# Kernel optimization log

Measured on AMD Instinct MI355X. Metric: run time of the kernel, lower is better.

## Reference

```python
import jax, jax.numpy as jnp
import numpy as np

H = 2048      # hidden_dim
OUT = 8       # output_dim
DICT = 50000  # dict_len (DND capacity)
FDIM = 6      # function_dim
RDIM = 1      # rule_dim
IN = FDIM + RDIM + OUT + 1  # input_dim = 16
NG = 5        # N_GATES
EPS = 1e-8


def setup_inputs() -> dict:
    key = jax.random.key(0)
    ks = jax.random.split(key, 16)
    f = lambda i, shape, s=1.0: jax.random.normal(ks[i], shape, jnp.float32) * s
    return {
        "x_t": f(0, (1, IN)),
        "h": f(1, (1, 1, H), 0.1),
        "c": f(2, (1, 1, H), 0.1),
        "W_i2h": f(3, ((NG + 1) * H, IN), 0.05),
        "b_i2h": jnp.zeros(((NG + 1) * H,), jnp.float32),
        "W_h2h": f(4, ((NG + 1) * H, H), 0.02),
        "b_h2h": jnp.zeros(((NG + 1) * H,), jnp.float32),
        "f_keys": f(5, (DICT, FDIM)),
        "f_vals": f(6, (DICT, H), 0.1),
        "r_keys": f(7, (DICT, RDIM)),
        "r_vals": f(8, (DICT, H), 0.1),
        "W_ih": f(9, (H, H), 0.02),
        "b_ih": jnp.zeros((H,), jnp.float32),
        "W_actor": f(10, (OUT, H), 0.02),
        "b_actor": jnp.zeros((OUT,), jnp.float32),
        "W_critic": f(11, (1, H), 0.02),
        "b_critic": jnp.zeros((1,), jnp.float32),
        "write_idx": 12345,
    }


def _dnd_read(q, keys, vals):
    # cosine similarity between query q [d] and all keys [N, d], softmax policy,
    # weighted sum over stored values [N, H] -> [H]
    qn = q / (jnp.linalg.norm(q) + EPS)
    kn = keys / (jnp.linalg.norm(keys, axis=1, keepdims=True) + EPS)
    sim = kn @ qn                      # [N]
    w = jax.nn.softmax(sim)            # [N]
    return w @ vals                    # [H]


def reference(x_t, h, c, W_i2h, b_i2h, W_h2h, b_h2h,
              f_keys, f_vals, r_keys, r_vals,
              W_ih, b_ih, W_actor, b_actor, W_critic, b_critic,
              write_idx):
    h2 = h.reshape(1, H)
    c2 = c.reshape(1, H)

    # fused gate preactivations: [1, 6H]
    preact = x_t @ W_i2h.T + b_i2h + h2 @ W_h2h.T + b_h2h
    gates = jax.nn.sigmoid(preact[:, :NG * H])
    f_t = gates[:, 0 * H:1 * H]
    i_t = gates[:, 1 * H:2 * H]
    o_t = gates[:, 2 * H:3 * H]
    fun_t = gates[:, 3 * H:4 * H]
    rul_t = gates[:, 4 * H:5 * H]
    c_new = jnp.tanh(preact[:, NG * H:])

    c_t = f_t * c2 + i_t * c_new

    # DND content-addressable reads (cosine sim + softmax over memory slots)
    q_f = x_t[0, :FDIM]
    q_r = x_t[0, FDIM:FDIM + RDIM]
    memfun_t = jnp.tanh(_dnd_read(q_f, f_keys, f_vals))  # [H]
    memrul_t = jnp.tanh(_dnd_read(q_r, r_keys, r_vals))  # [H]

    c_t = c_t + fun_t * memfun_t + rul_t * memrul_t
    h_t = o_t * jnp.tanh(c_t)

    # memory write (no-grad in original): function half / rule half of c_t
    c_ft = jax.lax.stop_gradient(c_t[0].at[H // 2:].set(0.0))
    c_rt = jax.lax.stop_gradient(c_t[0].at[:H // 2].set(0.0))
    new_f_keys = f_keys.at[write_idx].set(q_f)
    new_f_vals = f_vals.at[write_idx].set(c_ft)
    new_r_keys = r_keys.at[write_idx].set(q_r)
    new_r_vals = r_vals.at[write_idx].set(c_rt)

    # A2C head: shared relu layer, actor softmax, critic scalar
    ha = jax.nn.relu(h_t @ W_ih.T + b_ih)
    pi_a_t = jax.nn.softmax(ha @ W_actor.T + b_actor, axis=-1)  # [1, OUT]
    v_t = ha @ W_critic.T + b_critic                            # [1, 1]

    h_out = h_t.reshape(1, 1, H)
    c_out = c_t.reshape(1, 1, H)
    return (pi_a_t, v_t, h_out, c_out,
            new_f_keys, new_f_vals, new_r_keys, new_r_vals)
```

## Files before the change

### kernel.cpp

```cpp
#include <hip/hip_runtime.h>
#include <math.h>

#define H        2048
#define HD       12288
#define DICT     50000
#define FDIM     6
#define RDIM     1
#define IN_DIM   16
#define EPS_F    1e-8f

#define OFF_PI   ((size_t)0)
#define OFF_V    ((size_t)8)
#define OFF_H    ((size_t)9)
#define OFF_C    ((size_t)2057)
#define OFF_FK   ((size_t)4105)
#define OFF_FV   ((size_t)304105)
#define OFF_RK   ((size_t)102704105)
#define OFF_RV   ((size_t)102754105)

struct F4U { float x, y, z, w; };

__device__ __forceinline__ float sigf(float v) { return 1.0f / (1.0f + expf(-v)); }

__global__ void k_zero(float* __restrict__ p, int n) {
    int i = blockIdx.x * 256 + threadIdx.x;
    if (i < n) p[i] = 0.0f;
}

__global__ __launch_bounds__(256) void k_preact(
    const float* __restrict__ W_h2h, const float* __restrict__ W_i2h,
    const float* __restrict__ b_h2h, const float* __restrict__ b_i2h,
    const float* __restrict__ h, const float* __restrict__ x,
    float* __restrict__ preact)
{
    int gid  = blockIdx.x * blockDim.x + threadIdx.x;
    int row  = gid >> 6;
    int lane = threadIdx.x & 63;
    if (row >= HD) return;
    const float4* Wv = (const float4*)(W_h2h + (size_t)row * H);
    const float4* hv = (const float4*)h;
    float acc = 0.0f;
#pragma unroll
    for (int k = 0; k < 8; ++k) {
        float4 w4 = Wv[lane + (k << 6)];
        float4 h4 = hv[lane + (k << 6)];
        acc += w4.x * h4.x + w4.y * h4.y + w4.z * h4.z + w4.w * h4.w;
    }
    if (lane < IN_DIM) acc += W_i2h[(size_t)row * IN_DIM + lane] * x[lane];
#pragma unroll
    for (int off = 32; off > 0; off >>= 1) acc += __shfl_down(acc, off);
    if (lane == 0) preact[row] = acc + b_h2h[row] + b_i2h[row];
}

__global__ __launch_bounds__(256) void k_sims(
    const float* __restrict__ f_keys, const float* __restrict__ r_keys,
    const float* __restrict__ x,
    float* __restrict__ ef, float* __restrict__ er,
    float* __restrict__ sums,
    float* __restrict__ out_fk, float* __restrict__ out_rk)
{
    __shared__ float red[4];
    const int i    = blockIdx.x * 256 + threadIdx.x;
    const int dict = blockIdx.y;
    float e = 0.0f;

    if (dict == 0) {
        float qn[FDIM]; float qs = 0.0f;
        for (int d = 0; d < FDIM; ++d) { float q = x[d]; qn[d] = q; qs += q * q; }
        float qi = 1.0f / (sqrtf(qs) + EPS_F);
        if (i < DICT) {
            float ks = 0.0f, dot = 0.0f;
            for (int d = 0; d < FDIM; ++d) {
                float kv = f_keys[(size_t)i * FDIM + d];
                out_fk[(size_t)i * FDIM + d] = kv;
                ks += kv * kv; dot += kv * qn[d];
            }
            float sim = (dot * qi) / (sqrtf(ks) + EPS_F);
            e = expf(sim);
            ef[i] = e;
        }
    } else {
        float q  = x[FDIM];
        float qn = q / (fabsf(q) + EPS_F);
        if (i < DICT) {
            float kv = r_keys[i];
            out_rk[i] = kv;
            float sim = (kv * qn) / (fabsf(kv) + EPS_F);
            e = expf(sim);
            er[i] = e;
        }
    }
#pragma unroll
    for (int off = 32; off > 0; off >>= 1) e += __shfl_down(e, off);
    if ((threadIdx.x & 63) == 0) red[threadIdx.x >> 6] = e;
    __syncthreads();
    if (threadIdx.x == 0)
        atomicAdd(&sums[dict], red[0] + red[1] + red[2] + red[3]);
}

#define ROWS_PER_CHUNK 125
__global__ __launch_bounds__(256) void k_copy_wsum(
    const float* __restrict__ f_vals, const float* __restrict__ r_vals,
    const float* __restrict__ wf, const float* __restrict__ wr,
    float* __restrict__ out_fv, float* __restrict__ out_rv,
    float* __restrict__ memfun, float* __restrict__ memrul)
{
    __shared__ float wl[ROWS_PER_CHUNK];
    const int tid    = threadIdx.x;
    const int chunk  = blockIdx.x;
    const int stripe = blockIdx.y;
    const int dict   = blockIdx.z;

    const float* vals = dict ? r_vals : f_vals;
    const float* w    = dict ? wr     : wf;
    float*       outv = dict ? out_rv : out_fv;
    float*       mem  = dict ? memrul : memfun;

    const int row0 = chunk * ROWS_PER_CHUNK;
    if (tid < ROWS_PER_CHUNK) wl[tid] = w[row0 + tid];
    __syncthreads();

    const int colf = stripe * 256 + tid;
    const float4* vv = (const float4*)vals;
    F4U*          ov = (F4U*)outv;

    float ax = 0.f, ay = 0.f, az = 0.f, aw = 0.f;
    size_t base = (size_t)row0 * 512 + colf;
#pragma unroll 5
    for (int i = 0; i < ROWS_PER_CHUNK; ++i) {
        float4 v = vv[base];
        F4U s; s.x = v.x; s.y = v.y; s.z = v.z; s.w = v.w;
        ov[base] = s;
        float wv = wl[i];
        ax += wv * v.x; ay += wv * v.y; az += wv * v.z; aw += wv * v.w;
        base += 512;
    }
    const int c = colf * 4;
    atomicAdd(&mem[c + 0], ax);
    atomicAdd(&mem[c + 1], ay);
    atomicAdd(&mem[c + 2], az);
    atomicAdd(&mem[c + 3], aw);
}

__global__ __launch_bounds__(256) void k_combine(
    const float* __restrict__ preact, const float* __restrict__ c_in,
    const float* __restrict__ memfun, const float* __restrict__ memrul,
    const float* __restrict__ sums,
    const float* __restrict__ x, const int* __restrict__ widx_p,
    float* __restrict__ out, float* __restrict__ ht_ws)
{
    const int j = blockIdx.x * 256 + threadIdx.x;
    if (j >= H) return;
    const int widx = *widx_p;
    const float invf = 1.0f / sums[0];
    const float invr = 1.0f / sums[1];

    float f_t   = sigf(preact[0 * H + j]);
    float i_t   = sigf(preact[1 * H + j]);
    float o_t   = sigf(preact[2 * H + j]);
    float fun_t = sigf(preact[3 * H + j]);
    float rul_t = sigf(preact[4 * H + j]);
    float c_new = tanhf(preact[5 * H + j]);

    float ct = f_t * c_in[j] + i_t * c_new
             + fun_t * tanhf(memfun[j] * invf) + rul_t * tanhf(memrul[j] * invr);
    float ht = o_t * tanhf(ct);

    out[OFF_H + j] = ht;
    out[OFF_C + j] = ct;
    ht_ws[j] = ht;

    out[OFF_FV + (size_t)widx * H + j] = (j < H / 2) ? ct : 0.0f;
    out[OFF_RV + (size_t)widx * H + j] = (j < H / 2) ? 0.0f : ct;
    if (j < FDIM)  out[OFF_FK + (size_t)widx * FDIM + j] = x[j];
    if (j == FDIM) out[OFF_RK + (size_t)widx] = x[FDIM];
}

__global__ __launch_bounds__(256) void k_hidden(
    const float* __restrict__ W_ih, const float* __restrict__ b_ih,
    const float* __restrict__ ht, float* __restrict__ ha)
{
    int gid  = blockIdx.x * blockDim.x + threadIdx.x;
    int row  = gid >> 6;
    int lane = threadIdx.x & 63;
    if (row >= H) return;
    const float4* Wv = (const float4*)(W_ih + (size_t)row * H);
    const float4* hv = (const float4*)ht;
    float acc = 0.0f;
#pragma unroll
    for (int k = 0; k < 8; ++k) {
        float4 w4 = Wv[lane + (k << 6)];
        float4 h4 = hv[lane + (k << 6)];
        acc += w4.x * h4.x + w4.y * h4.y + w4.z * h4.z + w4.w * h4.w;
    }
#pragma unroll
    for (int off = 32; off > 0; off >>= 1) acc += __shfl_down(acc, off);
    if (lane == 0) ha[row] = fmaxf(acc + b_ih[row], 0.0f);
}

__global__ __launch_bounds__(256) void k_heads(
    const float* __restrict__ W_actor, const float* __restrict__ b_actor,
    const float* __restrict__ W_critic, const float* __restrict__ b_critic,
    const float* __restrict__ ha, float* __restrict__ out)
{
    __shared__ float red[4];
    __shared__ float logits[9];
    const int tid = threadIdx.x;

    for (int o = 0; o < 9; ++o) {
        const float* row = (o < 8) ? (W_actor + (size_t)o * H) : W_critic;
        float acc = 0.0f;
        for (int k = tid; k < H; k += 256) acc += row[k] * ha[k];
#pragma unroll
        for (int off = 32; off > 0; off >>= 1) acc += __shfl_down(acc, off);
        if ((tid & 63) == 0) red[tid >> 6] = acc;
        __syncthreads();
        if (tid == 0)
            logits[o] = red[0] + red[1] + red[2] + red[3] + ((o < 8) ? b_actor[o] : b_critic[0]);
        __syncthreads();
    }
    if (tid == 0) {
        float m = logits[0];
        for (int o = 1; o < 8; ++o) m = fmaxf(m, logits[o]);
        float e[8], s = 0.0f;
        for (int o = 0; o < 8; ++o) { e[o] = expf(logits[o] - m); s += e[o]; }
        for (int o = 0; o < 8; ++o) out[OFF_PI + o] = e[o] / s;
        out[OFF_V] = logits[8];
    }
}

extern "C" void kernel_launch(void* const* d_in, const int* in_sizes, int n_in,
                              void* d_out, int out_size, void* d_ws, size_t ws_size,
                              hipStream_t stream)
{
    const float* x        = (const float*)d_in[0];
    const float* h        = (const float*)d_in[1];
    const float* c        = (const float*)d_in[2];
    const float* W_i2h    = (const float*)d_in[3];
    const float* b_i2h    = (const float*)d_in[4];
    const float* W_h2h    = (const float*)d_in[5];
    const float* b_h2h    = (const float*)d_in[6];
    const float* f_keys   = (const float*)d_in[7];
    const float* f_vals   = (const float*)d_in[8];
    const float* r_keys   = (const float*)d_in[9];
    const float* r_vals   = (const float*)d_in[10];
    const float* W_ih     = (const float*)d_in[11];
    const float* b_ih     = (const float*)d_in[12];
    const float* W_actor  = (const float*)d_in[13];
    const float* b_actor  = (const float*)d_in[14];
    const float* W_critic = (const float*)d_in[15];
    const float* b_critic = (const float*)d_in[16];
    const int*   widx     = (const int*)d_in[17];

    float* out = (float*)d_out;
    float* ws  = (float*)d_ws;

    float* preact = ws;
    float* ef     = ws + 12288;
    float* er     = ws + 62288;
    float* memfun = ws + 112288;
    float* memrul = ws + 114336;
    float* sums   = ws + 116384;
    float* ht_ws  = ws + 116392;
    float* ha     = ws + 118440;

    k_zero<<<17, 256, 0, stream>>>(memfun, 2 * H + 2);

    k_preact<<<HD / 4, 256, 0, stream>>>(W_h2h, W_i2h, b_h2h, b_i2h, h, x, preact);

    k_sims<<<dim3((DICT + 255) / 256, 2), 256, 0, stream>>>(
        f_keys, r_keys, x, ef, er, sums, out + OFF_FK, out + OFF_RK);

    k_copy_wsum<<<dim3(DICT / ROWS_PER_CHUNK, 2, 2), 256, 0, stream>>>(
        f_vals, r_vals, ef, er, out + OFF_FV, out + OFF_RV, memfun, memrul);

    k_combine<<<H / 256, 256, 0, stream>>>(preact, c, memfun, memrul, sums, x, widx, out, ht_ws);

    k_hidden<<<H / 4, 256, 0, stream>>>(W_ih, b_ih, ht_ws, ha);
    k_heads<<<1, 256, 0, stream>>>(W_actor, b_actor, W_critic, b_critic, ha, out);
}
```

Measured before the change: 461.2 us.

## Fuse preact, similarity, and value copy-weighted-sum into one kernel

Merges the gate preactivation GEMV, the DND key similarity/exp computation, and the value-table copy plus weighted sum into a single launch. Each value block now computes its own 125 exp weights locally, so the ef/er workspace round-trip is gone. The preact rows run in the same grid as separate blocks and can overlap with the bandwidth-bound copy. Value loads and stores now use nontemporal hints, and each block covers a full row width with 512 threads instead of splitting it across stripes.

Result: no change. 454.4 us (-1.5%).

```diff
diff --git a/kernel.cpp b/kernel.cpp
--- a/kernel.cpp
+++ b/kernel.cpp
@@ -18,7 +18,13 @@
 #define OFF_RK   ((size_t)102704105)
 #define OFF_RV   ((size_t)102754105)
 
-struct F4U { float x, y, z, w; };
+#define R_CHUNK      125
+#define NBLK_DICT    (DICT / R_CHUNK)
+#define NBLK_VALS    (2 * NBLK_DICT)
+#define NBLK_PREACT  (HD / 8)
+#define NBLK_TOTAL   (NBLK_VALS + NBLK_PREACT)
+
+typedef float f4v __attribute__((ext_vector_type(4)));
 
 __device__ __forceinline__ float sigf(float v) { return 1.0f / (1.0f + expf(-v)); }
 
@@ -27,119 +33,120 @@
     if (i < n) p[i] = 0.0f;
 }
 
-__global__ __launch_bounds__(256) void k_preact(
+__global__ __launch_bounds__(512) void k_mega(
+    const float* __restrict__ f_keys, const float* __restrict__ r_keys,
+    const float* __restrict__ f_vals, const float* __restrict__ r_vals,
+    const float* __restrict__ x,
     const float* __restrict__ W_h2h, const float* __restrict__ W_i2h,
     const float* __restrict__ b_h2h, const float* __restrict__ b_i2h,
-    const float* __restrict__ h, const float* __restrict__ x,
-    float* __restrict__ preact)
-{
-    int gid  = blockIdx.x * blockDim.x + threadIdx.x;
-    int row  = gid >> 6;
-    int lane = threadIdx.x & 63;
-    if (row >= HD) return;
-    const float4* Wv = (const float4*)(W_h2h + (size_t)row * H);
-    const float4* hv = (const float4*)h;
-    float acc = 0.0f;
-#pragma unroll
-    for (int k = 0; k < 8; ++k) {
-        float4 w4 = Wv[lane + (k << 6)];
-        float4 h4 = hv[lane + (k << 6)];
-        acc += w4.x * h4.x + w4.y * h4.y + w4.z * h4.z + w4.w * h4.w;
-    }
-    if (lane < IN_DIM) acc += W_i2h[(size_t)row * IN_DIM + lane] * x[lane];
-#pragma unroll
-    for (int off = 32; off > 0; off >>= 1) acc += __shfl_down(acc, off);
-    if (lane == 0) preact[row] = acc + b_h2h[row] + b_i2h[row];
-}
-
-__global__ __launch_bounds__(256) void k_sims(
-    const float* __restrict__ f_keys, const float* __restrict__ r_keys,
-    const float* __restrict__ x,
-    float* __restrict__ ef, float* __restrict__ er,
-    float* __restrict__ sums,
-    float* __restrict__ out_fk, float* __restrict__ out_rk)
-{
-    __shared__ float red[4];
-    const int i    = blockIdx.x * 256 + threadIdx.x;
-    const int dict = blockIdx.y;
-    float e = 0.0f;
-
-    if (dict == 0) {
-        float qn[FDIM]; float qs = 0.0f;
-        for (int d = 0; d < FDIM; ++d) { float q = x[d]; qn[d] = q; qs += q * q; }
-        float qi = 1.0f / (sqrtf(qs) + EPS_F);
-        if (i < DICT) {
+    const float* __restrict__ h,
+    float* __restrict__ out_fv, float* __restrict__ out_rv,
+    float* __restrict__ out_fk, float* __restrict__ out_rk,
+    float* __restrict__ memfun, float* __restrict__ memrul,
+    float* __restrict__ sums, float* __restrict__ preact)
+{
+    const int b   = blockIdx.x;
+    const int tid = threadIdx.x;
+
+    if (b >= NBLK_VALS) {
+        const int row  = (b - NBLK_VALS) * 8 + (tid >> 6);
+        const int lane = tid & 63;
+        const float4* Wv = (const float4*)(W_h2h + (size_t)row * H);
+        const float4* hv = (const float4*)h;
+        float acc = 0.0f;
+#pragma unroll
+        for (int k = 0; k < 8; ++k) {
+            float4 w4 = Wv[lane + (k << 6)];
+            float4 h4 = hv[lane + (k << 6)];
+            acc += w4.x * h4.x + w4.y * h4.y + w4.z * h4.z + w4.w * h4.w;
+        }
+        if (lane < IN_DIM) acc += W_i2h[(size_t)row * IN_DIM + lane] * x[lane];
+#pragma unroll
+        for (int off = 32; off > 0; off >>= 1) acc += __shfl_down(acc, off);
+        if (lane == 0) preact[row] = acc + b_h2h[row] + b_i2h[row];
+        return;
+    }
+
+    __shared__ float wl[R_CHUNK];
+    const int  dict = (b >= NBLK_DICT) ? 1 : 0;
+    const int  row0 = (dict ? b - NBLK_DICT : b) * R_CHUNK;
+
+    const float* vals = dict ? r_vals : f_vals;
+    float*       outv = dict ? out_rv : out_fv;
+    float*       mem  = dict ? memrul : memfun;
+
+    if (!dict) {
+        for (int i = tid; i < R_CHUNK * FDIM; i += 512)
+            out_fk[(size_t)row0 * FDIM + i] = f_keys[(size_t)row0 * FDIM + i];
+    } else if (tid < R_CHUNK) {
+        out_rk[row0 + tid] = r_keys[row0 + tid];
+    }
+
+    if (tid < R_CHUNK) {
+        const int row = row0 + tid;
+        float e;
+        if (!dict) {
+            float qn[FDIM]; float qs = 0.0f;
+#pragma unroll
+            for (int d = 0; d < FDIM; ++d) { float q = x[d]; qn[d] = q; qs += q * q; }
+            const float qi = 1.0f / (sqrtf(qs) + EPS_F);
             float ks = 0.0f, dot = 0.0f;
+#pragma unroll
             for (int d = 0; d < FDIM; ++d) {
-                float kv = f_keys[(size_t)i * FDIM + d];
-                out_fk[(size_t)i * FDIM + d] = kv;
+                float kv = f_keys[(size_t)row * FDIM + d];
                 ks += kv * kv; dot += kv * qn[d];
             }
-            float sim = (dot * qi) / (sqrtf(ks) + EPS_F);
-            e = expf(sim);
-            ef[i] = e;
+            e = expf((dot * qi) / (sqrtf(ks) + EPS_F));
+        } else {
+            float q  = x[FDIM];
+            float kv = r_keys[row];
+            e = expf((kv * (q / (fabsf(q) + EPS_F))) / (fabsf(kv) + EPS_F));
         }
-    } else {
-        float q  = x[FDIM];
-        float qn = q / (fabsf(q) + EPS_F);
-        if (i < DICT) {
-            float kv = r_keys[i];
-            out_rk[i] = kv;
-            float sim = (kv * qn) / (fabsf(kv) + EPS_F);
-            e = expf(sim);
-            er[i] = e;
-        }
-    }
-#pragma unroll
-    for (int off = 32; off > 0; off >>= 1) e += __shfl_down(e, off);
-    if ((threadIdx.x & 63) == 0) red[threadIdx.x >> 6] = e;
+        wl[tid] = e;
+    }
     __syncthreads();
-    if (threadIdx.x == 0)
-        atomicAdd(&sums[dict], red[0] + red[1] + red[2] + red[3]);
-}
-
-#define ROWS_PER_CHUNK 125
-__global__ __launch_bounds__(256) void k_copy_wsum(
-    const float* __restrict__ f_vals, const float* __restrict__ r_vals,
-    const float* __restrict__ wf, const float* __restrict__ wr,
-    float* __restrict__ out_fv, float* __restrict__ out_rv,
-    float* __restrict__ memfun, float* __restrict__ memrul)
-{
-    __shared__ float wl[ROWS_PER_CHUNK];
-    const int tid    = threadIdx.x;
-    const int chunk  = blockIdx.x;
-    const int stripe = blockIdx.y;
-    const int dict   = blockIdx.z;
-
-    const float* vals = dict ? r_vals : f_vals;
-    const float* w    = dict ? wr     : wf;
-    float*       outv = dict ? out_rv : out_fv;
-    float*       mem  = dict ? memrul : memfun;
-
-    const int row0 = chunk * ROWS_PER_CHUNK;
-    if (tid < ROWS_PER_CHUNK) wl[tid] = w[row0 + tid];
-    __syncthreads();
-
-    const int colf = stripe * 256 + tid;
-    const float4* vv = (const float4*)vals;
-    F4U*          ov = (F4U*)outv;
-
-    float ax = 0.f, ay = 0.f, az = 0.f, aw = 0.f;
-    size_t base = (size_t)row0 * 512 + colf;
-#pragma unroll 5
-    for (int i = 0; i < ROWS_PER_CHUNK; ++i) {
-        float4 v = vv[base];
-        F4U s; s.x = v.x; s.y = v.y; s.z = v.z; s.w = v.w;
-        ov[base] = s;
-        float wv = wl[i];
-        ax += wv * v.x; ay += wv * v.y; az += wv * v.z; aw += wv * v.w;
-        base += 512;
-    }
-    const int c = colf * 4;
-    atomicAdd(&mem[c + 0], ax);
-    atomicAdd(&mem[c + 1], ay);
-    atomicAdd(&mem[c + 2], az);
-    atomicAdd(&mem[c + 3], aw);
+    if (tid == 0) {
+        float s = 0.0f;
+        for (int i = 0; i < R_CHUNK; ++i) s += wl[i];
+        atomicAdd(&sums[dict], s);
+    }
+
+    const f4v* vv = (const f4v*)vals;
+    float a0 = 0.f, a1 = 0.f, a2 = 0.f, a3 = 0.f;
+    size_t base = (size_t)row0 * 512 + tid;
+    for (int i0 = 0; i0 < R_CHUNK; i0 += 5) {
+        f4v v0 = __builtin_nontemporal_load(&vv[base]);
+        f4v v1 = __builtin_nontemporal_load(&vv[base +  512]);
+        f4v v2 = __builtin_nontemporal_load(&vv[base + 1024]);
+        f4v v3 = __builtin_nontemporal_load(&vv[base + 1536]);
+        f4v v4 = __builtin_nontemporal_load(&vv[base + 2048]);
+        const float w0 = wl[i0], w1 = wl[i0+1], w2 = wl[i0+2], w3 = wl[i0+3], w4 = wl[i0+4];
+        a0 += w0*v0.x + w1*v1.x + w2*v2.x + w3*v3.x + w4*v4.x;
+        a1 += w0*v0.y + w1*v1.y + w2*v2.y + w3*v3.y + w4*v4.y;
+        a2 += w0*v0.z + w1*v1.z + w2*v2.z + w3*v3.z + w4*v4.z;
+        a3 += w0*v0.w + w1*v1.w + w2*v2.w + w3*v3.w + w4*v4.w;
+        float* o0 = outv + (base        ) * 4;
+        float* o1 = outv + (base +  512 ) * 4;
+        float* o2 = outv + (base + 1024 ) * 4;
+        float* o3 = outv + (base + 1536 ) * 4;
+        float* o4 = outv + (base + 2048 ) * 4;
+        __builtin_nontemporal_store(v0.x, o0+0); __builtin_nontemporal_store(v0.y, o0+1);
+        __builtin_nontemporal_store(v0.z, o0+2); __builtin_nontemporal_store(v0.w, o0+3);
+        __builtin_nontemporal_store(v1.x, o1+0); __builtin_nontemporal_store(v1.y, o1+1);
+        __builtin_nontemporal_store(v1.z, o1+2); __builtin_nontemporal_store(v1.w, o1+3);
+        __builtin_nontemporal_store(v2.x, o2+0); __builtin_nontemporal_store(v2.y, o2+1);
+        __builtin_nontemporal_store(v2.z, o2+2); __builtin_nontemporal_store(v2.w, o2+3);
+        __builtin_nontemporal_store(v3.x, o3+0); __builtin_nontemporal_store(v3.y, o3+1);
+        __builtin_nontemporal_store(v3.z, o3+2); __builtin_nontemporal_store(v3.w, o3+3);
+        __builtin_nontemporal_store(v4.x, o4+0); __builtin_nontemporal_store(v4.y, o4+1);
+        __builtin_nontemporal_store(v4.z, o4+2); __builtin_nontemporal_store(v4.w, o4+3);
+        base += 5 * 512;
+    }
+    const int c = tid * 4;
+    atomicAdd(&mem[c + 0], a0);
+    atomicAdd(&mem[c + 1], a1);
+    atomicAdd(&mem[c + 2], a2);
+    atomicAdd(&mem[c + 3], a3);
 }
 
 __global__ __launch_bounds__(256) void k_combine(
@@ -256,23 +263,19 @@
     float* ws  = (float*)d_ws;
 
     float* preact = ws;
-    float* ef     = ws + 12288;
-    float* er     = ws + 62288;
-    float* memfun = ws + 112288;
-    float* memrul = ws + 114336;
-    float* sums   = ws + 116384;
-    float* ht_ws  = ws + 116392;
-    float* ha     = ws + 118440;
+    float* memfun = ws + 12288;
+    float* memrul = ws + 14336;
+    float* sums   = ws + 16384;
+    float* ht_ws  = ws + 16388;
+    float* ha     = ws + 18436;
 
     k_zero<<<17, 256, 0, stream>>>(memfun, 2 * H + 2);
 
-    k_preact<<<HD / 4, 256, 0, stream>>>(W_h2h, W_i2h, b_h2h, b_i2h, h, x, preact);
-
-    k_sims<<<dim3((DICT + 255) / 256, 2), 256, 0, stream>>>(
-        f_keys, r_keys, x, ef, er, sums, out + OFF_FK, out + OFF_RK);
-
-    k_copy_wsum<<<dim3(DICT / ROWS_PER_CHUNK, 2, 2), 256, 0, stream>>>(
-        f_vals, r_vals, ef, er, out + OFF_FV, out + OFF_RV, memfun, memrul);
+    k_mega<<<NBLK_TOTAL, 512, 0, stream>>>(
+        f_keys, r_keys, f_vals, r_vals, x,
+        W_h2h, W_i2h, b_h2h, b_i2h, h,
+        out + OFF_FV, out + OFF_RV, out + OFF_FK, out + OFF_RK,
+        memfun, memrul, sums, preact);
 
     k_combine<<<H / 256, 256, 0, stream>>>(preact, c, memfun, memrul, sums, x, widx, out, ht_ws);
 
```

## Replace value copy-and-weighted-sum with aligned persistent grid-stride sweep

Applied to the files above, without the earlier changes.

Replaces the chunked copy/weighted-sum kernel with a persistent 800-block grid-stride sweep. It reads each value table as contiguous float4 vectors offset by three floats, so stores into the output (which starts at an odd float offset) become 16-byte aligned. Each thread keeps a fixed column group, so one set of atomics per thread still works. The few leading and trailing elements are handled separately. It also splits the heads kernel into a 9-block dot-product kernel plus a tiny softmax kernel, and reorders launches. The aim is to cut unaligned-store and write traffic overhead on the roughly 800MB copy, at the cost of more complex indexing and unaligned loads.

After: 564.6 us. +22.4%, slower.

```diff
diff --git a/kernel.cpp b/kernel.cpp
--- a/kernel.cpp
+++ b/kernel.cpp
@@ -18,38 +18,19 @@
 #define OFF_RK   ((size_t)102704105)
 #define OFF_RV   ((size_t)102754105)
 
-struct F4U { float x, y, z, w; };
+#define NBLK_SWEEP  800
+#define NTH         (NBLK_SWEEP * 512)
+#define PH_FLOATS   ((long long)DICT * H)
+#define QPH         ((PH_FLOATS - 4) / 4)
+
+typedef float f4v  __attribute__((ext_vector_type(4)));
+typedef f4v  f4vu  __attribute__((aligned(4)));
 
 __device__ __forceinline__ float sigf(float v) { return 1.0f / (1.0f + expf(-v)); }
 
 __global__ void k_zero(float* __restrict__ p, int n) {
     int i = blockIdx.x * 256 + threadIdx.x;
     if (i < n) p[i] = 0.0f;
-}
-
-__global__ __launch_bounds__(256) void k_preact(
-    const float* __restrict__ W_h2h, const float* __restrict__ W_i2h,
-    const float* __restrict__ b_h2h, const float* __restrict__ b_i2h,
-    const float* __restrict__ h, const float* __restrict__ x,
-    float* __restrict__ preact)
-{
-    int gid  = blockIdx.x * blockDim.x + threadIdx.x;
-    int row  = gid >> 6;
-    int lane = threadIdx.x & 63;
-    if (row >= HD) return;
-    const float4* Wv = (const float4*)(W_h2h + (size_t)row * H);
-    const float4* hv = (const float4*)h;
-    float acc = 0.0f;
-#pragma unroll
-    for (int k = 0; k < 8; ++k) {
-        float4 w4 = Wv[lane + (k << 6)];
-        float4 h4 = hv[lane + (k << 6)];
-        acc += w4.x * h4.x + w4.y * h4.y + w4.z * h4.z + w4.w * h4.w;
-    }
-    if (lane < IN_DIM) acc += W_i2h[(size_t)row * IN_DIM + lane] * x[lane];
-#pragma unroll
-    for (int off = 32; off > 0; off >>= 1) acc += __shfl_down(acc, off);
-    if (lane == 0) preact[row] = acc + b_h2h[row] + b_i2h[row];
 }
 
 __global__ __launch_bounds__(256) void k_sims(
@@ -66,17 +47,18 @@
 
     if (dict == 0) {
         float qn[FDIM]; float qs = 0.0f;
+#pragma unroll
         for (int d = 0; d < FDIM; ++d) { float q = x[d]; qn[d] = q; qs += q * q; }
         float qi = 1.0f / (sqrtf(qs) + EPS_F);
         if (i < DICT) {
             float ks = 0.0f, dot = 0.0f;
+#pragma unroll
             for (int d = 0; d < FDIM; ++d) {
                 float kv = f_keys[(size_t)i * FDIM + d];
                 out_fk[(size_t)i * FDIM + d] = kv;
                 ks += kv * kv; dot += kv * qn[d];
             }
-            float sim = (dot * qi) / (sqrtf(ks) + EPS_F);
-            e = expf(sim);
+            e = expf((dot * qi) / (sqrtf(ks) + EPS_F));
             ef[i] = e;
         }
     } else {
@@ -85,8 +67,7 @@
         if (i < DICT) {
             float kv = r_keys[i];
             out_rk[i] = kv;
-            float sim = (kv * qn) / (fabsf(kv) + EPS_F);
-            e = expf(sim);
+            e = expf((kv * qn) / (fabsf(kv) + EPS_F));
             er[i] = e;
         }
     }
@@ -98,48 +79,84 @@
         atomicAdd(&sums[dict], red[0] + red[1] + red[2] + red[3]);
 }
 
-#define ROWS_PER_CHUNK 125
-__global__ __launch_bounds__(256) void k_copy_wsum(
+__global__ __launch_bounds__(256) void k_preact(
+    const float* __restrict__ W_h2h, const float* __restrict__ W_i2h,
+    const float* __restrict__ b_h2h, const float* __restrict__ b_i2h,
+    const float* __restrict__ h, const float* __restrict__ x,
+    float* __restrict__ preact)
+{
+    int gid  = blockIdx.x * blockDim.x + threadIdx.x;
+    int row  = gid >> 6;
+    int lane = threadIdx.x & 63;
+    if (row >= HD) return;
+    const float4* Wv = (const float4*)(W_h2h + (size_t)row * H);
+    const float4* hv = (const float4*)h;
+    float acc = 0.0f;
+#pragma unroll
+    for (int k = 0; k < 8; ++k) {
+        float4 w4 = Wv[lane + (k << 6)];
+        float4 h4 = hv[lane + (k << 6)];
+        acc += w4.x * h4.x + w4.y * h4.y + w4.z * h4.z + w4.w * h4.w;
+    }
+    if (lane < IN_DIM) acc += W_i2h[(size_t)row * IN_DIM + lane] * x[lane];
+#pragma unroll
+    for (int off = 32; off > 0; off >>= 1) acc += __shfl_down(acc, off);
+    if (lane == 0) preact[row] = acc + b_h2h[row] + b_i2h[row];
+}
+
+__device__ __forceinline__ void sweep_phase(
+    const float* __restrict__ src, float* __restrict__ dst,
+    const float* __restrict__ w, float* __restrict__ mem, int g)
+{
+    const long long f0 = 4LL * g + 3;
+    const int  c0 = (int)(f0 & 2047);
+    int        r  = (int)(f0 >> 11);
+    long long  fo = f0;
+    float a0 = 0.f, a1 = 0.f, a2 = 0.f, a3 = 0.f;
+
+    if (c0 != 2047) {
+        for (long long k = g; k < QPH; k += NTH, fo += 4LL * NTH, r += NBLK_SWEEP) {
+            f4vu v = *(const f4vu*)(src + fo);
+            const float wr = w[r];
+            a0 += wr * v.x; a1 += wr * v.y; a2 += wr * v.z; a3 += wr * v.w;
+            *(f4v*)(dst + fo) = v;
+        }
+        atomicAdd(&mem[c0 + 0], a0);
+        atomicAdd(&mem[c0 + 1], a1);
+        atomicAdd(&mem[c0 + 2], a2);
+        atomicAdd(&mem[c0 + 3], a3);
+    } else {
+        for (long long k = g; k < QPH; k += NTH, fo += 4LL * NTH, r += NBLK_SWEEP) {
+            f4vu v = *(const f4vu*)(src + fo);
+            const float wr = w[r], wn = w[r + 1];
+            a0 += wr * v.x; a1 += wn * v.y; a2 += wn * v.z; a3 += wn * v.w;
+            *(f4v*)(dst + fo) = v;
+        }
+        atomicAdd(&mem[2047], a0);
+        atomicAdd(&mem[0],    a1);
+        atomicAdd(&mem[1],    a2);
+        atomicAdd(&mem[2],    a3);
+    }
+    if (g == 0) {
+        float s0 = src[0], s1 = src[1], s2 = src[2], sl = src[PH_FLOATS - 1];
+        dst[0] = s0; dst[1] = s1; dst[2] = s2; dst[PH_FLOATS - 1] = sl;
+        const float w0 = w[0], wl = w[DICT - 1];
+        atomicAdd(&mem[0],    w0 * s0);
+        atomicAdd(&mem[1],    w0 * s1);
+        atomicAdd(&mem[2],    w0 * s2);
+        atomicAdd(&mem[2047], wl * sl);
+    }
+}
+
+__global__ __launch_bounds__(512, 8) void k_sweep(
     const float* __restrict__ f_vals, const float* __restrict__ r_vals,
-    const float* __restrict__ wf, const float* __restrict__ wr,
+    const float* __restrict__ ef, const float* __restrict__ er,
     float* __restrict__ out_fv, float* __restrict__ out_rv,
     float* __restrict__ memfun, float* __restrict__ memrul)
 {
-    __shared__ float wl[ROWS_PER_CHUNK];
-    const int tid    = threadIdx.x;
-    const int chunk  = blockIdx.x;
-    const int stripe = blockIdx.y;
-    const int dict   = blockIdx.z;
-
-    const float* vals = dict ? r_vals : f_vals;
-    const float* w    = dict ? wr     : wf;
-    float*       outv = dict ? out_rv : out_fv;
-    float*       mem  = dict ? memrul : memfun;
-
-    const int row0 = chunk * ROWS_PER_CHUNK;
-    if (tid < ROWS_PER_CHUNK) wl[tid] = w[row0 + tid];
-    __syncthreads();
-
-    const int colf = stripe * 256 + tid;
-    const float4* vv = (const float4*)vals;
-    F4U*          ov = (F4U*)outv;
-
-    float ax = 0.f, ay = 0.f, az = 0.f, aw = 0.f;
-    size_t base = (size_t)row0 * 512 + colf;
-#pragma unroll 5
-    for (int i = 0; i < ROWS_PER_CHUNK; ++i) {
-        float4 v = vv[base];
-        F4U s; s.x = v.x; s.y = v.y; s.z = v.z; s.w = v.w;
-        ov[base] = s;
-        float wv = wl[i];
-        ax += wv * v.x; ay += wv * v.y; az += wv * v.z; aw += wv * v.w;
-        base += 512;
-    }
-    const int c = colf * 4;
-    atomicAdd(&mem[c + 0], ax);
-    atomicAdd(&mem[c + 1], ay);
-    atomicAdd(&mem[c + 2], az);
-    atomicAdd(&mem[c + 3], aw);
+    const int g = blockIdx.x * 512 + threadIdx.x;
+    sweep_phase(f_vals, out_fv, ef, memfun, g);
+    sweep_phase(r_vals, out_rv, er, memrul, g);
 }
 
 __global__ __launch_bounds__(256) void k_combine(
@@ -198,28 +215,37 @@
     if (lane == 0) ha[row] = fmaxf(acc + b_ih[row], 0.0f);
 }
 
-__global__ __launch_bounds__(256) void k_heads(
+__global__ __launch_bounds__(256) void k_heads1(
     const float* __restrict__ W_actor, const float* __restrict__ b_actor,
     const float* __restrict__ W_critic, const float* __restrict__ b_critic,
-    const float* __restrict__ ha, float* __restrict__ out)
+    const float* __restrict__ ha, float* __restrict__ logits)
 {
     __shared__ float red[4];
-    __shared__ float logits[9];
+    const int o   = blockIdx.x;
     const int tid = threadIdx.x;
-
-    for (int o = 0; o < 9; ++o) {
-        const float* row = (o < 8) ? (W_actor + (size_t)o * H) : W_critic;
-        float acc = 0.0f;
-        for (int k = tid; k < H; k += 256) acc += row[k] * ha[k];
-#pragma unroll
-        for (int off = 32; off > 0; off >>= 1) acc += __shfl_down(acc, off);
-        if ((tid & 63) == 0) red[tid >> 6] = acc;
-        __syncthreads();
-        if (tid == 0)
-            logits[o] = red[0] + red[1] + red[2] + red[3] + ((o < 8) ? b_actor[o] : b_critic[0]);
-        __syncthreads();
-    }
-    if (tid == 0) {
+    const float* row = (o < 8) ? (W_actor + (size_t)o * H) : W_critic;
+    const float4* rv = (const float4*)row;
+    const float4* hv = (const float4*)ha;
+    float acc = 0.0f;
+#pragma unroll
+    for (int k = 0; k < 2; ++k) {
+        int idx = tid + (k << 8);
+        float4 w4 = rv[idx];
+        float4 h4 = hv[idx];
+        acc += w4.x * h4.x + w4.y * h4.y + w4.z * h4.z + w4.w * h4.w;
+    }
+#pragma unroll
+    for (int off = 32; off > 0; off >>= 1) acc += __shfl_down(acc, off);
+    if ((tid & 63) == 0) red[tid >> 6] = acc;
+    __syncthreads();
+    if (tid == 0)
+        logits[o] = red[0] + red[1] + red[2] + red[3] + ((o < 8) ? b_actor[o] : b_critic[0]);
+}
+
+__global__ __launch_bounds__(64) void k_heads2(
+    const float* __restrict__ logits, float* __restrict__ out)
+{
+    if (threadIdx.x == 0) {
         float m = logits[0];
         for (int o = 1; o < 8; ++o) m = fmaxf(m, logits[o]);
         float e[8], s = 0.0f;
@@ -263,19 +289,21 @@
     float* sums   = ws + 116384;
     float* ht_ws  = ws + 116392;
     float* ha     = ws + 118440;
+    float* logits = ws + 120488;
 
     k_zero<<<17, 256, 0, stream>>>(memfun, 2 * H + 2);
-
-    k_preact<<<HD / 4, 256, 0, stream>>>(W_h2h, W_i2h, b_h2h, b_i2h, h, x, preact);
 
     k_sims<<<dim3((DICT + 255) / 256, 2), 256, 0, stream>>>(
         f_keys, r_keys, x, ef, er, sums, out + OFF_FK, out + OFF_RK);
 
-    k_copy_wsum<<<dim3(DICT / ROWS_PER_CHUNK, 2, 2), 256, 0, stream>>>(
+    k_preact<<<HD / 4, 256, 0, stream>>>(W_h2h, W_i2h, b_h2h, b_i2h, h, x, preact);
+
+    k_sweep<<<NBLK_SWEEP, 512, 0, stream>>>(
         f_vals, r_vals, ef, er, out + OFF_FV, out + OFF_RV, memfun, memrul);
 
     k_combine<<<H / 256, 256, 0, stream>>>(preact, c, memfun, memrul, sums, x, widx, out, ht_ws);
 
     k_hidden<<<H / 4, 256, 0, stream>>>(W_ih, b_ih, ht_ws, ha);
-    k_heads<<<1, 256, 0, stream>>>(W_actor, b_actor, W_critic, b_critic, ha, out);
-}
+    k_heads1<<<9, 256, 0, stream>>>(W_actor, b_actor, W_critic, b_critic, ha, logits);
+    k_heads2<<<1, 64, 0, stream>>>(logits, out);
+}
```
